# Kernel tuning notes

Hardware: AMD Instinct MI355X
Metric: run time of the kernel (lower is better)

## Reference

```python
import jax, jax.numpy as jnp
import numpy as np

T = 2048; HIDDEN = 2048; HQ = 32; G = 2; D = 64
KERNEL = 32; STRIDE = 16; BLOCK = 64; TOPK = 16
INIT_BLOCKS = 1; LOCAL_BLOCKS = 2; WINDOW = 512
ROPE_BASE = 10000.0
NEG = -1e30


def _rope(x):
    # x: [T, H, D], non-interleaved rotate-half rope
    t, h, d = x.shape
    half = d // 2
    inv = 1.0 / (ROPE_BASE ** (jnp.arange(half, dtype=jnp.float32) / half))
    freqs = jnp.arange(t, dtype=jnp.float32)[:, None] * inv[None, :]
    cos = jnp.cos(freqs)[:, None, :]
    sin = jnp.sin(freqs)[:, None, :]
    x1, x2 = x[..., :half], x[..., half:]
    return jnp.concatenate([x1 * cos - x2 * sin, x2 * cos + x1 * sin], axis=-1)


def setup_inputs() -> dict:
    key = jax.random.key(0)
    ks = jax.random.split(key, 8)
    s = 0.02
    return {
        "hidden_states": jax.random.normal(ks[0], (1, T, HIDDEN), jnp.float32),
        "Wq": jax.random.normal(ks[1], (HQ * D, HIDDEN), jnp.float32) * s,
        "Wk": jax.random.normal(ks[2], (G * D, HIDDEN), jnp.float32) * s,
        "Wv": jax.random.normal(ks[3], (G * D, HIDDEN), jnp.float32) * s,
        "Wo": jax.random.normal(ks[4], (HIDDEN, HQ * D), jnp.float32) * s,
        "Wgate": jax.random.normal(ks[5], (3, HIDDEN), jnp.float32) * s,
        "compress_key": jax.random.normal(ks[6], (G, D * KERNEL, D), jnp.float32) * s,
        "compress_value": jax.random.normal(ks[7], (G, D * KERNEL, D), jnp.float32) * s,
    }


def reference(hidden_states, Wq, Wk, Wv, Wo, Wgate, compress_key, compress_value):
    x = hidden_states[0]                      # [T, HIDDEN] (single varlen sequence)
    scale = 1.0 / np.sqrt(D).astype(np.float32)
    q = (x @ Wq.T).reshape(T, HQ, D)
    k = (x @ Wk.T).reshape(T, G, D)
    v = (x @ Wv.T).reshape(T, G, D)
    gate = jax.nn.sigmoid(x @ Wgate.T)        # [T, 3]
    q = _rope(q)
    k = _rope(k)

    # --- branch 1: compressed attention (linear_compress + compressed_attention) ---
    C = (T - KERNEL) // STRIDE + 1            # compressed sequence length
    starts = jnp.arange(C) * STRIDE
    win_idx = starts[:, None] + jnp.arange(KERNEL)[None, :]        # [C, KERNEL]
    kw = k[win_idx].transpose(2, 0, 1, 3).reshape(G, C, KERNEL * D)
    vw = v[win_idx].transpose(2, 0, 1, 3).reshape(G, C, KERNEL * D)
    ck = jnp.einsum('gcf,gfd->cgd', kw, compress_key)              # [C, G, D]
    cv = jnp.einsum('gcf,gfd->cgd', vw, compress_value)

    qg = q.reshape(T, G, HQ // G, D)          # [T, G, group, D]
    cs = jnp.einsum('tghd,cgd->ghtc', qg, ck) * scale              # [G, grp, T, C]
    # query i may attend compressed token j iff i >= j*stride + kernel - 1
    cmask = jnp.arange(T)[:, None] >= (starts + KERNEL - 1)[None, :]  # [T, C]
    cs = jnp.where(cmask[None, None], cs, NEG)
    p = jax.nn.softmax(cs, axis=-1)
    valid = cmask.any(-1)                     # queries with >=1 compressed key
    p = jnp.where(valid[None, None, :, None], p, 0.0)
    comp_out = jnp.einsum('ghtc,cgd->tghd', p, cv).reshape(T, HQ, D)

    # --- topk block selection from pooled compressed attention scores ---
    NB = T // BLOCK
    bstart = jnp.arange(NB) * BLOCK
    # compressed token j overlaps key block b
    overlap = ((starts[:, None] < bstart[None, :] + BLOCK) &
               (starts[:, None] + KERNEL > bstart[None, :])).astype(p.dtype)  # [C, NB]
    score = jnp.einsum('ghtc,cb->gtb', p, overlap)                 # [G, T, NB]
    qblock = jnp.arange(T) // BLOCK
    b = jnp.arange(NB)
    causal_b = b[None, :] <= qblock[:, None]                       # [T, NB]
    forced = (b[None, :] < INIT_BLOCKS) | (((qblock[:, None] - b[None, :]) < LOCAL_BLOCKS) & causal_b)
    score = jnp.where(forced[None], jnp.inf, score)
    score = jnp.where(causal_b[None], score, -jnp.inf)
    _, topk_idx = jax.lax.top_k(score, TOPK)                       # [G, T, TOPK]
    tk_valid = jnp.take_along_axis(score, topk_idx, axis=-1) > -jnp.inf
    sel = ((topk_idx[..., None] == b) & tk_valid[..., None]).any(axis=2)  # [G, T, NB]

    # --- branch 2: topk block-sparse attention ---
    key_block = jnp.arange(T) // BLOCK
    keymask = sel[:, :, key_block]                                 # [G, T, Tk]
    causal = jnp.arange(T)[:, None] >= jnp.arange(T)[None, :]      # [T, Tk]
    smask = keymask & causal[None]
    ss = jnp.einsum('tghd,sgd->ghts', qg, k) * scale               # [G, grp, T, Tk]
    ss = jnp.where(smask[:, None], ss, NEG)
    sparse_out = jnp.einsum('ghts,sgd->tghd', jax.nn.softmax(ss, -1), v).reshape(T, HQ, D)

    # --- branch 3: sliding window attention (causal, left window) ---
    delta = jnp.arange(T)[:, None] - jnp.arange(T)[None, :]
    wmask = (delta >= 0) & (delta <= WINDOW)                       # [T, Tk]
    ws = jnp.einsum('tghd,sgd->ghts', qg, k) * scale
    ws = jnp.where(wmask[None, None], ws, NEG)
    slide_out = jnp.einsum('ghts,sgd->tghd', jax.nn.softmax(ws, -1), v).reshape(T, HQ, D)

    # --- learned gate fusion + output projection ---
    out = (gate[:, 0, None, None] * comp_out +
           gate[:, 1, None, None] * sparse_out +
           gate[:, 2, None, None] * slide_out)                    # [T, HQ, D]
    o = out.reshape(T, HQ * D) @ Wo.T
    return o[None]                                                 # [1, T, HIDDEN]
```

## Files before the change

### kernel.cpp

```cpp
#include <hip/hip_runtime.h>
#include <math.h>

#define T_SEQ 2048
#define NHQ 32
#define NG 2
#define HD 64
#define CSTRIDE 16
#define KVGW 384

typedef __attribute__((ext_vector_type(8))) short short8_t;
typedef __attribute__((ext_vector_type(4))) short short4_t;
typedef __attribute__((ext_vector_type(4))) float f32x4;

__device__ __forceinline__ ushort f2bf(float x) {
  union { float f; unsigned u; } c; c.f = x;
  unsigned r = c.u + 0x7fff + ((c.u >> 16) & 1);
  return (ushort)(r >> 16);
}
__device__ __forceinline__ float bf2f(ushort u) {
  union { unsigned u; float f; } c; c.u = ((unsigned)u) << 16;
  return c.f;
}

__device__ __forceinline__ void glds16(const ushort* g, ushort* l) {
  __builtin_amdgcn_global_load_lds(
      (const __attribute__((address_space(1))) unsigned int*)g,
      (__attribute__((address_space(3))) unsigned int*)l, 16, 0, 0);
}

__global__ __launch_bounds__(256) void mgemm(
    const ushort* __restrict__ A, const ushort* __restrict__ B,
    float* __restrict__ C, int M, int N, int K) {
  __shared__ __align__(16) ushort As[128 * 64];
  __shared__ __align__(16) ushort Bs[64 * 64];
  const int tid = threadIdx.x;
  const int lane = tid & 63, w = tid >> 6;
  const int quad = lane >> 4, l16 = lane & 15;
  const int m0 = blockIdx.y * 128, n0 = blockIdx.x * 64;
  const int mq = (w & 1) * 64, nq = (w >> 1) * 32;
  f32x4 acc[4][2];
  const f32x4 fz = {0.f, 0.f, 0.f, 0.f};
  #pragma unroll
  for (int i = 0; i < 4; ++i)
    #pragma unroll
    for (int j = 0; j < 2; ++j) acc[i][j] = fz;

  for (int k0 = 0; k0 < K; k0 += 64) {
    __syncthreads();
    #pragma unroll
    for (int j = 0; j < 4; ++j) {
      int ci = j * 256 + tid;
      int row = ci >> 3, cl = ci & 7;
      int kc = cl ^ (row & 7);
      glds16(A + ((size_t)(m0 + row) * K + k0 + kc * 8), &As[ci * 8]);
    }
    #pragma unroll
    for (int j = 0; j < 2; ++j) {
      int ci = j * 256 + tid;
      int row = ci >> 3, cl = ci & 7;
      int kc = cl ^ (row & 7);
      glds16(B + ((size_t)(n0 + row) * K + k0 + kc * 8), &Bs[ci * 8]);
    }
    __syncthreads();
    #pragma unroll
    for (int kt = 0; kt < 2; ++kt) {
      short8_t af[4], bf_[2];
      #pragma unroll
      for (int mt = 0; mt < 4; ++mt) {
        int row = mq + mt * 16 + l16;
        int cl = (kt * 4 + quad) ^ (row & 7);
        af[mt] = *(const short8_t*)&As[row * 64 + cl * 8];
      }
      #pragma unroll
      for (int nt = 0; nt < 2; ++nt) {
        int row = nq + nt * 16 + l16;
        int cl = (kt * 4 + quad) ^ (row & 7);
        bf_[nt] = *(const short8_t*)&Bs[row * 64 + cl * 8];
      }
      #pragma unroll
      for (int mt = 0; mt < 4; ++mt)
        #pragma unroll
        for (int nt = 0; nt < 2; ++nt)
          acc[mt][nt] = __builtin_amdgcn_mfma_f32_16x16x32_bf16(
              af[mt], bf_[nt], acc[mt][nt], 0, 0, 0);
    }
  }
  #pragma unroll
  for (int mt = 0; mt < 4; ++mt)
    #pragma unroll
    for (int nt = 0; nt < 2; ++nt)
      #pragma unroll
      for (int r = 0; r < 4; ++r) {
        int m = m0 + mq + mt * 16 + quad * 4 + r;
        int n = n0 + nq + nt * 16 + l16;
        C[(size_t)m * N + n] = acc[mt][nt][r];
      }
}

__global__ __launch_bounds__(256) void cvt_bf(const float* __restrict__ src,
                                              ushort* __restrict__ dst, int n) {
  int i = (blockIdx.x * 256 + threadIdx.x) * 4;
  if (i >= n) return;
  float4 v = *(const float4*)(src + i);
  short4_t o = {(short)f2bf(v.x), (short)f2bf(v.y),
                (short)f2bf(v.z), (short)f2bf(v.w)};
  *(short4_t*)(dst + i) = o;
}

__global__ __launch_bounds__(256) void cvt_sum2_bf(const float* __restrict__ a,
                                                   const float* __restrict__ b,
                                                   ushort* __restrict__ dst, int n) {
  int i = (blockIdx.x * 256 + threadIdx.x) * 4;
  if (i >= n) return;
  float4 va = *(const float4*)(a + i);
  float4 vb = *(const float4*)(b + i);
  short4_t o = {(short)f2bf(va.x + vb.x), (short)f2bf(va.y + vb.y),
                (short)f2bf(va.z + vb.z), (short)f2bf(va.w + vb.w)};
  *(short4_t*)(dst + i) = o;
}

__global__ __launch_bounds__(256) void pack_wkvg(
    const float* __restrict__ Wk, const float* __restrict__ Wv,
    const float* __restrict__ Wg, ushort* __restrict__ dst) {
  int i = blockIdx.x * 256 + threadIdx.x;
  if (i >= KVGW * 2048) return;
  int n = i >> 11, k = i & 2047;
  float v;
  if (n < 128) v = Wk[(size_t)n * 2048 + k];
  else if (n < 256) v = Wv[(size_t)(n - 128) * 2048 + k];
  else if (n < 259) v = Wg[(size_t)(n - 256) * 2048 + k];
  else v = 0.f;
  dst[i] = f2bf(v);
}

__global__ __launch_bounds__(256) void cvt_vt(const float* __restrict__ kvg,
                                              ushort* __restrict__ vt) {
  int i = blockIdx.x * 256 + threadIdx.x;
  if (i >= T_SEQ * NG * HD) return;
  int d = i & 63, g = (i >> 6) & 1, s = i >> 7;
  int blk = s >> 6, k = s & 63;
  int snew = blk * 64 + (((k >> 2) ^ (d & 15)) << 2) + (k & 3);
  vt[((size_t)g * HD + d) * T_SEQ + snew] =
      f2bf(kvg[(size_t)s * KVGW + 128 + g * 64 + d]);
}

__global__ __launch_bounds__(256) void rope_all(
    const float* __restrict__ q, float* __restrict__ kvg,
    ushort* __restrict__ qbf, ushort* __restrict__ kbf) {
  const int t = blockIdx.x;
  const float lnb_over = 9.210340371976184f / 32.f;
  for (int job = threadIdx.x; job < (NHQ + NG) * 32; job += 256) {
    int h = job >> 5, j = job & 31;
    float inv = expf(-(float)j * lnb_over);
    float fr = (float)t * inv;
    float c_ = cosf(fr), s_ = sinf(fr);
    if (h < NHQ) {
      const float cq = c_ * 0.125f, sq = s_ * 0.125f;
      const float* base = q + ((size_t)t * NHQ + h) * HD;
      float x1 = base[j], x2 = base[j + 32];
      ushort* ob = qbf + ((size_t)t * NHQ + h) * HD;
      ob[j] = f2bf(x1 * cq - x2 * sq);
      ob[j + 32] = f2bf(x2 * cq + x1 * sq);
    } else {
      int g = h - NHQ;
      float* base = kvg + (size_t)t * KVGW + g * 64;
      float x1 = base[j], x2 = base[j + 32];
      float o1 = x1 * c_ - x2 * s_, o2 = x2 * c_ + x1 * s_;
      base[j] = o1; base[j + 32] = o2;
      kbf[(size_t)t * 128 + g * 64 + j] = f2bf(o1);
      kbf[(size_t)t * 128 + g * 64 + j + 32] = f2bf(o2);
    }
  }
}

__global__ __launch_bounds__(256) void compress_kv(
    const float* __restrict__ kvg,
    const float* __restrict__ Wck, const float* __restrict__ Wcv,
    ushort* __restrict__ ck16, ushort* __restrict__ cvt16) {
  const int c = blockIdx.x, g = blockIdx.y;
  const int tid = threadIdx.x;
  if (c == 127) {
    if (tid < 64) ck16[((size_t)127 * NG + g) * HD + tid] = 0;
    else if (tid < 128) cvt16[((size_t)g * HD + (tid - 64)) * 128 + 127] = 0;
    return;
  }
  const int d = tid & 63, chunk = tid >> 6;
  __shared__ float red[2][4][64];
  float ak = 0.f, av = 0.f;
  #pragma unroll 4
  for (int f = chunk * 512; f < chunk * 512 + 512; ++f) {
    int i = f >> 6, e = f & 63;
    int trow = c * CSTRIDE + i;
    float kv = kvg[(size_t)trow * KVGW + g * 64 + e];
    float vv = kvg[(size_t)trow * KVGW + 128 + g * 64 + e];
    ak += kv * Wck[((size_t)g * 2048 + f) * HD + d];
    av += vv * Wcv[((size_t)g * 2048 + f) * HD + d];
  }
  red[0][chunk][d] = ak;
  red[1][chunk][d] = av;
  __syncthreads();
  if (tid < 64) {
    ck16[((size_t)c * NG + g) * HD + tid] =
        f2bf(red[0][0][tid] + red[0][1][tid] + red[0][2][tid] + red[0][3][tid]);
  } else if (tid < 128) {
    int dd = tid - 64;
    cvt16[((size_t)g * HD + dd) * 128 + c] =
        f2bf(red[1][0][dd] + red[1][1][dd] + red[1][2][dd] + red[1][3][dd]);
  }
}

__global__ __launch_bounds__(512) void comp_attn(
    const ushort* __restrict__ qbf, const ushort* __restrict__ ck16,
    const ushort* __restrict__ cvt16, const float* __restrict__ kvg,
    float* __restrict__ comb, unsigned* __restrict__ sel) {
  const int tb = 127 - blockIdx.x, g = blockIdx.y;
  const int t0 = tb * 16;
  const int tid = threadIdx.x, lane = tid & 63, w = tid >> 6;
  const int quad = lane >> 4, l16 = lane & 15;
  const int qb = t0 >> 6;

  __shared__ float colsum[16][129];
  for (int i = tid; i < 16 * 129; i += 512) ((float*)colsum)[i] = 0.f;
  __syncthreads();

  const int t = t0 + l16;
  const int cmaxv = (t >= 31) ? min(126, (t - 31) >> 4) : -1;
  const int h0 = w * 2;

  short8_t qB[2][2];
  #pragma unroll
  for (int hh = 0; hh < 2; ++hh)
    #pragma unroll
    for (int kd = 0; kd < 2; ++kd)
      qB[hh][kd] = *(const short8_t*)(qbf +
          ((size_t)t * NHQ + g * 16 + h0 + hh) * HD + kd * 32 + quad * 8);

  const f32x4 fz = {0.f, 0.f, 0.f, 0.f};
  f32x4 sp[2][8];

  #pragma unroll
  for (int ct = 0; ct < 8; ++ct) {
    const ushort* kr = ck16 + ((size_t)(ct * 16 + l16) * NG + g) * HD + quad * 8;
    short8_t kA0 = *(const short8_t*)kr;
    short8_t kA1 = *(const short8_t*)(kr + 32);
    #pragma unroll
    for (int hh = 0; hh < 2; ++hh) {
      f32x4 c0 = __builtin_amdgcn_mfma_f32_16x16x32_bf16(kA0, qB[hh][0], fz, 0, 0, 0);
      sp[hh][ct] = __builtin_amdgcn_mfma_f32_16x16x32_bf16(kA1, qB[hh][1], c0, 0, 0, 0);
    }
  }

  short4_t pB[2][8];
  #pragma unroll
  for (int hh = 0; hh < 2; ++hh) {
    float mx = -INFINITY;
    #pragma unroll
    for (int ct = 0; ct < 8; ++ct)
      #pragma unroll
      for (int r = 0; r < 4; ++r) {
        int c = ct * 16 + quad * 4 + r;
        float s_ = (c <= cmaxv) ? sp[hh][ct][r] : -INFINITY;
        sp[hh][ct][r] = s_;
        mx = fmaxf(mx, s_);
      }
    mx = fmaxf(mx, __shfl_xor(mx, 16));
    mx = fmaxf(mx, __shfl_xor(mx, 32));
    if (mx == -INFINITY) mx = 0.f;
    float ls = 0.f;
    #pragma unroll
    for (int ct = 0; ct < 8; ++ct)
      #pragma unroll
      for (int r = 0; r < 4; ++r) {
        float p = __expf(sp[hh][ct][r] - mx);
        sp[hh][ct][r] = p;
        ls += p;
      }
    ls += __shfl_xor(ls, 16);
    ls += __shfl_xor(ls, 32);
    float inv = (ls > 0.f) ? 1.f / ls : 0.f;
    #pragma unroll
    for (int ct = 0; ct < 8; ++ct) {
      short4_t pk;
      #pragma unroll
      for (int r = 0; r < 4; ++r) {
        float pn = sp[hh][ct][r] * inv;
        sp[hh][ct][r] = pn;
        pk[r] = (short)f2bf(pn);
      }
      pB[hh][ct] = pk;
    }
  }

  #pragma unroll
  for (int ct = 0; ct < 8; ++ct)
    #pragma unroll
    for (int r = 0; r < 4; ++r)
      atomicAdd(&colsum[l16][ct * 16 + quad * 4 + r],
                sp[0][ct][r] + sp[1][ct][r]);

  f32x4 acc[2][4];
  #pragma unroll
  for (int hh = 0; hh < 2; ++hh)
    #pragma unroll
    for (int dt = 0; dt < 4; ++dt) acc[hh][dt] = fz;
  #pragma unroll
  for (int ct = 0; ct < 8; ++ct) {
    short4_t vA[4];
    #pragma unroll
    for (int dt = 0; dt < 4; ++dt)
      vA[dt] = *(const short4_t*)(cvt16 +
          ((size_t)g * HD + dt * 16 + l16) * 128 + ct * 16 + quad * 4);
    #pragma unroll
    for (int hh = 0; hh < 2; ++hh)
      #pragma unroll
      for (int dt = 0; dt < 4; ++dt)
        acc[hh][dt] = __builtin_amdgcn_mfma_f32_16x16x16bf16_1k(
            vA[dt], pB[hh][ct], acc[hh][dt], 0, 0, 0);
  }

  const float g0 = 1.f / (1.f + __expf(-kvg[(size_t)t * KVGW + 256]));
  #pragma unroll
  for (int hh = 0; hh < 2; ++hh)
    #pragma unroll
    for (int dt = 0; dt < 4; ++dt)
      #pragma unroll
      for (int r = 0; r < 4; ++r)
        comb[((size_t)t * NHQ + g * 16 + h0 + hh) * HD + dt * 16 + quad * 4 + r] =
            g0 * acc[hh][dt][r];

  __syncthreads();

  {
    const int tl = tid >> 5;
    const int b = tid & 31;
    float s;
    if (b > qb) s = -INFINITY;
    else if (b == 0 || qb - b < 2) s = INFINITY;
    else {
      s = 0.f;
      #pragma unroll
      for (int i = 0; i < 5; ++i) s += colsum[tl][4 * b - 1 + i];
    }
    unsigned key = (s < 0.f) ? 0u : (__float_as_uint(s) + 1u);
    unsigned msel = 0;
    for (int it = 0; it < 16; ++it) {
      unsigned long long pk =
          (((unsigned long long)key) << 6) | (unsigned)(63 - b);
      #pragma unroll
      for (int off = 16; off >= 1; off >>= 1) {
        unsigned long long o = __shfl_xor(pk, off);
        if (o > pk) pk = o;
      }
      if ((pk >> 6) == 0) break;
      int bs = 63 - (int)(pk & 63);
      msel |= 1u << bs;
      if (b == bs) key = 0;
    }
    if (b == 0) sel[(size_t)(t0 + tl) * NG + g] = msel;
  }
}

__global__ __launch_bounds__(512, 2) void mfma_attn(
    const ushort* __restrict__ qb16, const ushort* __restrict__ kb16,
    const ushort* __restrict__ vtb, const float* __restrict__ kvg,
    const unsigned* __restrict__ sel, float* __restrict__ comb2) {
  const int qb = 31 - blockIdx.x, g = blockIdx.y;
  const int hgp = blockIdx.z;
  const int tid = threadIdx.x, lane = tid & 63, w = tid >> 6;
  const int quad = lane >> 4, l16 = lane & 15;
  const int head = g * 16 + hgp * 2 + (w >> 2);
  const int t0 = qb * 64;

  __shared__ __align__(16) ushort Ks[2][64 * 64];
  __shared__ __align__(16) ushort Vs[2][64 * 64];
  __shared__ unsigned sel_s[64];

  if (tid < 64) sel_s[tid] = sel[(size_t)(t0 + tid) * NG + g];
  __syncthreads();

  const int qg = t0 + (w & 3) * 16 + l16;
  const unsigned sbq = sel_s[(w & 3) * 16 + l16];

  short8_t qB0 = *(const short8_t*)(qb16 +
      ((size_t)qg * NHQ + head) * HD + quad * 8);
  short8_t qB1 = *(const short8_t*)(qb16 +
      ((size_t)qg * NHQ + head) * HD + 32 + quad * 8);

  float m0 = -1e30f, m1 = -1e30f;
  f32x4 acc0[4], acc1[4], accL0, accL1;
  const f32x4 fz = {0.f, 0.f, 0.f, 0.f};
  #pragma unroll
  for (int dt = 0; dt < 4; ++dt) { acc0[dt] = fz; acc1[dt] = fz; }
  accL0 = fz; accL1 = fz;
  const short4_t onesA = {(short)0x3F80, (short)0x3F80,
                          (short)0x3F80, (short)0x3F80};

  unsigned uni = sel_s[lane];
  #pragma unroll
  for (int off = 32; off >= 1; off >>= 1) uni |= __shfl_xor(uni, off);
  const int b0w = (qb > 8) ? qb - 8 : 0;
  const unsigned wmask = ((1u << (qb - b0w + 1)) - 1u) << b0w;
  unsigned lrem = uni | wmask;
  const int nb = __popc(lrem);

  #define STAGE(buf, blk)                                                     \
    {                                                                         \
      const int blk_ = (blk);                                                 \
      const int row = tid >> 3, cl = tid & 7;                                 \
      const int kck = cl ^ (row & 7);                                         \
      glds16(kb16 + (size_t)(blk_ * 64 + row) * 128 + g * 64 + kck * 8,       \
             &Ks[buf][tid * 8]);                                              \
      glds16(vtb + ((size_t)g * 64 + row) * 2048 + blk_ * 64 + cl * 8,        \
             &Vs[buf][tid * 8]);                                              \
    }

  int blkcur = __ffs(lrem) - 1; lrem &= lrem - 1;
  STAGE(0, blkcur);
  __syncthreads();

  const int e = l16 & 7;

  for (int ib = 0; ib < nb; ++ib) {
    const int cur = ib & 1;
    const int blk = blkcur;
    if (ib + 1 < nb) {
      blkcur = __ffs(lrem) - 1; lrem &= lrem - 1;
      STAGE(cur ^ 1, blkcur);
    }

    f32x4 sp[4];
    __builtin_amdgcn_s_setprio(1);
    #pragma unroll
    for (int kt = 0; kt < 4; ++kt) {
      const ushort* kr = &Ks[cur][(kt * 16 + l16) * 64];
      short8_t kA0 = *(const short8_t*)(kr + ((quad ^ e) * 8));
      short8_t kA1 = *(const short8_t*)(kr + ((quad ^ e ^ 4) * 8));
      f32x4 c = __builtin_amdgcn_mfma_f32_16x16x32_bf16(kA0, qB0, fz, 0, 0, 0);
      sp[kt] = __builtin_amdgcn_mfma_f32_16x16x32_bf16(kA1, qB1, c, 0, 0, 0);
    }
    __builtin_amdgcn_s_setprio(0);

    const bool diag = (blk == qb);
    const bool wedge = (blk == qb - 8);
    const bool inU = ((uni >> blk) & 1u) != 0;
    const bool inW = ((wmask >> blk) & 1u) != 0;
    const bool selq = ((sbq >> blk) & 1u) != 0;

    float rm = -INFINITY;
    #pragma unroll
    for (int kt = 0; kt < 4; ++kt)
      #pragma unroll
      for (int r = 0; r < 4; ++r) rm = fmaxf(rm, sp[kt][r]);
    rm = fmaxf(rm, __shfl_xor(rm, 16));
    rm = fmaxf(rm, __shfl_xor(rm, 32));

    if (inU) {
      float mx;
      if (!diag) {
        mx = selq ? rm : -INFINITY;
      } else {
        mx = -INFINITY;
        #pragma unroll
        for (int kt = 0; kt < 4; ++kt)
          #pragma unroll
          for (int r = 0; r < 4; ++r) {
            int key = blk * 64 + kt * 16 + quad * 4 + r;
            bool ok = selq && (key <= qg);
            mx = ok ? fmaxf(mx, sp[kt][r]) : mx;
          }
        mx = fmaxf(mx, __shfl_xor(mx, 16));
        mx = fmaxf(mx, __shfl_xor(mx, 32));
      }
      if (!__all(mx <= m0 + 8.f)) {
        float mnew = fmaxf(m0, mx);
        float alpha = __expf(m0 - mnew);
        #pragma unroll
        for (int dt = 0; dt < 4; ++dt)
          #pragma unroll
          for (int r = 0; r < 4; ++r) acc0[dt][r] *= alpha;
        #pragma unroll
        for (int r = 0; r < 4; ++r) accL0[r] *= alpha;
        m0 = mnew;
      }
      short4_t pB[4];
      #pragma unroll
      for (int kt = 0; kt < 4; ++kt) {
        union { unsigned u[2]; short4_t s; } pk;
        if (!diag) {
          float p0 = __expf(sp[kt][0] - m0), p1 = __expf(sp[kt][1] - m0);
          float p2 = __expf(sp[kt][2] - m0), p3 = __expf(sp[kt][3] - m0);
          asm("v_cvt_pk_bf16_f32 %0, %1, %2" : "=v"(pk.u[0]) : "v"(p0), "v"(p1));
          asm("v_cvt_pk_bf16_f32 %0, %1, %2" : "=v"(pk.u[1]) : "v"(p2), "v"(p3));
          pk.u[0] = selq ? pk.u[0] : 0u;
          pk.u[1] = selq ? pk.u[1] : 0u;
        } else {
          float p[4];
          #pragma unroll
          for (int r = 0; r < 4; ++r) {
            int key = blk * 64 + kt * 16 + quad * 4 + r;
            bool ok = selq && (key <= qg);
            p[r] = ok ? __expf(sp[kt][r] - m0) : 0.f;
          }
          asm("v_cvt_pk_bf16_f32 %0, %1, %2" : "=v"(pk.u[0]) : "v"(p[0]), "v"(p[1]));
          asm("v_cvt_pk_bf16_f32 %0, %1, %2" : "=v"(pk.u[1]) : "v"(p[2]), "v"(p[3]));
        }
        pB[kt] = pk.s;
      }
      __builtin_amdgcn_s_setprio(1);
      #pragma unroll
      for (int kt = 0; kt < 4; ++kt) {
        #pragma unroll
        for (int dt = 0; dt < 4; ++dt) {
          short4_t vA = *(const short4_t*)(&Vs[cur][(dt * 16 + l16) * 64 +
                                                    (((kt * 4 + quad) ^ l16) << 2)]);
          acc0[dt] = __builtin_amdgcn_mfma_f32_16x16x16bf16_1k(
              vA, pB[kt], acc0[dt], 0, 0, 0);
        }
        accL0 = __builtin_amdgcn_mfma_f32_16x16x16bf16_1k(
            onesA, pB[kt], accL0, 0, 0, 0);
      }
      __builtin_amdgcn_s_setprio(0);
    }

    if (inW) {
      float mx;
      if (!diag && !wedge) {
        mx = rm;
      } else {
        mx = -INFINITY;
        #pragma unroll
        for (int kt = 0; kt < 4; ++kt)
          #pragma unroll
          for (int r = 0; r < 4; ++r) {
            int key = blk * 64 + kt * 16 + quad * 4 + r;
            bool ok = (key <= qg) && (qg - key <= 512);
            mx = ok ? fmaxf(mx, sp[kt][r]) : mx;
          }
        mx = fmaxf(mx, __shfl_xor(mx, 16));
        mx = fmaxf(mx, __shfl_xor(mx, 32));
      }
      if (!__all(mx <= m1 + 8.f)) {
        float mnew = fmaxf(m1, mx);
        float alpha = __expf(m1 - mnew);
        #pragma unroll
        for (int dt = 0; dt < 4; ++dt)
          #pragma unroll
          for (int r = 0; r < 4; ++r) acc1[dt][r] *= alpha;
        #pragma unroll
        for (int r = 0; r < 4; ++r) accL1[r] *= alpha;
        m1 = mnew;
      }
      short4_t pB[4];
      #pragma unroll
      for (int kt = 0; kt < 4; ++kt) {
        union { unsigned u[2]; short4_t s; } pk;
        if (!diag && !wedge) {
          float p0 = __expf(sp[kt][0] - m1), p1 = __expf(sp[kt][1] - m1);
          float p2 = __expf(sp[kt][2] - m1), p3 = __expf(sp[kt][3] - m1);
          asm("v_cvt_pk_bf16_f32 %0, %1, %2" : "=v"(pk.u[0]) : "v"(p0), "v"(p1));
          asm("v_cvt_pk_bf16_f32 %0, %1, %2" : "=v"(pk.u[1]) : "v"(p2), "v"(p3));
        } else {
          float p[4];
          #pragma unroll
          for (int r = 0; r < 4; ++r) {
            int key = blk * 64 + kt * 16 + quad * 4 + r;
            bool ok = (key <= qg) && (qg - key <= 512);
            p[r] = ok ? __expf(sp[kt][r] - m1) : 0.f;
          }
          asm("v_cvt_pk_bf16_f32 %0, %1, %2" : "=v"(pk.u[0]) : "v"(p[0]), "v"(p[1]));
          asm("v_cvt_pk_bf16_f32 %0, %1, %2" : "=v"(pk.u[1]) : "v"(p[2]), "v"(p[3]));
        }
        pB[kt] = pk.s;
      }
      __builtin_amdgcn_s_setprio(1);
      #pragma unroll
      for (int kt = 0; kt < 4; ++kt) {
        #pragma unroll
        for (int dt = 0; dt < 4; ++dt) {
          short4_t vA = *(const short4_t*)(&Vs[cur][(dt * 16 + l16) * 64 +
                                                    (((kt * 4 + quad) ^ l16) << 2)]);
          acc1[dt] = __builtin_amdgcn_mfma_f32_16x16x16bf16_1k(
              vA, pB[kt], acc1[dt], 0, 0, 0);
        }
        accL1 = __builtin_amdgcn_mfma_f32_16x16x16bf16_1k(
            onesA, pB[kt], accL1, 0, 0, 0);
      }
      __builtin_amdgcn_s_setprio(0);
    }

    __syncthreads();
  }
  #undef STAGE

  const float c0 =
      (1.f / (1.f + __expf(-kvg[(size_t)qg * KVGW + 257]))) / accL0[0];
  const float c1 =
      (1.f / (1.f + __expf(-kvg[(size_t)qg * KVGW + 258]))) / accL1[0];
  #pragma unroll
  for (int dt = 0; dt < 4; ++dt)
    #pragma unroll
    for (int r = 0; r < 4; ++r) {
      const int d = dt * 16 + quad * 4 + r;
      comb2[((size_t)qg * NHQ + head) * HD + d] =
          c0 * acc0[dt][r] + c1 * acc1[dt][r];
    }
}

extern "C" void kernel_launch(void* const* d_in, const int* in_sizes, int n_in,
                              void* d_out, int out_size, void* d_ws, size_t ws_size,
                              hipStream_t stream) {
  const float* x   = (const float*)d_in[0];
  const float* Wq  = (const float*)d_in[1];
  const float* Wk  = (const float*)d_in[2];
  const float* Wv  = (const float*)d_in[3];
  const float* Wo  = (const float*)d_in[4];
  const float* Wg  = (const float*)d_in[5];
  const float* Wck = (const float*)d_in[6];
  const float* Wcv = (const float*)d_in[7];
  float* out = (float*)d_out;
  float* ws = (float*)d_ws;

  float* qbuf   = ws;
  float* comb1  = qbuf + 4194304;
  float* kvg    = comb1 + 4194304;
  float* ckb    = kvg + 786432;
  float* cvb    = ckb + 16384;
  unsigned* sel = (unsigned*)(cvb + 16384);
  ushort* kbf   = (ushort*)(sel + 4096);
  ushort* vtb   = kbf + 262144;
  ushort* wkvgb = vtb + 262144;
  ushort* regA  = wkvgb + 786432;
  ushort* regB  = regA + 4194304;
  ushort* xb = regA;      ushort* combb = regA;
  ushort* wqb = regB;     ushort* qbf = regB;
  float* comb2 = qbuf;
  ushort* wob = (ushort*)qbuf;

  ushort* ckb16 = (ushort*)ckb;
  ushort* cvtb  = ckb16 + 16384;

  const int CV4 = (1048576 + 255) / 256;
  cvt_bf<<<CV4, 256, 0, stream>>>(x, xb, 4194304);
  cvt_bf<<<CV4, 256, 0, stream>>>(Wq, wqb, 4194304);
  pack_wkvg<<<(KVGW * 2048 + 255) / 256, 256, 0, stream>>>(Wk, Wv, Wg, wkvgb);

  mgemm<<<dim3(32, 16), 256, 0, stream>>>(xb, wqb, qbuf, 2048, 2048, 2048);
  mgemm<<<dim3(6, 16), 256, 0, stream>>>(xb, wkvgb, kvg, 2048, KVGW, 2048);

  rope_all<<<2048, 256, 0, stream>>>(qbuf, kvg, qbf, kbf);
  cvt_vt<<<(262144 + 255) / 256, 256, 0, stream>>>(kvg, vtb);
  compress_kv<<<dim3(128, 2), 256, 0, stream>>>(kvg, Wck, Wcv, ckb16, cvtb);
  comp_attn<<<dim3(128, 2), 512, 0, stream>>>(qbf, ckb16, cvtb, kvg, comb1, sel);
  mfma_attn<<<dim3(32, 2, 8), 512, 0, stream>>>(qbf, kbf, vtb, kvg, sel, comb2);

  cvt_sum2_bf<<<CV4, 256, 0, stream>>>(comb1, comb2, combb, 4194304);
  cvt_bf<<<CV4, 256, 0, stream>>>(Wo, wob, 4194304);
  mgemm<<<dim3(32, 16), 256, 0, stream>>>(combb, wob, out, 2048, 2048, 2048);
}
```

Before: 378.6 us.

## Fuse comb sum and bf16 cast into attention epilogue; use exp2 softmax

The attention kernel now reads the compressed-branch output, adds its own gated result and writes the bf16 combined tensor directly, which removes the separate cvt_sum2_bf pass and the fp32 comb2 round trip. The query scale is folded with log2(e) so every softmax exponent becomes exp2f, and the rescale threshold is widened to match the base-2 scale. The Wo conversion moves earlier in the stream, and half the head groups process query blocks in ascending order to balance causal work. The wider threshold slightly raises the risk of larger unnormalised accumulators.

```diff
diff --git a/kernel.cpp b/kernel.cpp
--- a/kernel.cpp
+++ b/kernel.cpp
@@ -107,18 +107,6 @@
   *(short4_t*)(dst + i) = o;
 }
 
-__global__ __launch_bounds__(256) void cvt_sum2_bf(const float* __restrict__ a,
-                                                   const float* __restrict__ b,
-                                                   ushort* __restrict__ dst, int n) {
-  int i = (blockIdx.x * 256 + threadIdx.x) * 4;
-  if (i >= n) return;
-  float4 va = *(const float4*)(a + i);
-  float4 vb = *(const float4*)(b + i);
-  short4_t o = {(short)f2bf(va.x + vb.x), (short)f2bf(va.y + vb.y),
-                (short)f2bf(va.z + vb.z), (short)f2bf(va.w + vb.w)};
-  *(short4_t*)(dst + i) = o;
-}
-
 __global__ __launch_bounds__(256) void pack_wkvg(
     const float* __restrict__ Wk, const float* __restrict__ Wv,
     const float* __restrict__ Wg, ushort* __restrict__ dst) {
@@ -149,13 +137,14 @@
     ushort* __restrict__ qbf, ushort* __restrict__ kbf) {
   const int t = blockIdx.x;
   const float lnb_over = 9.210340371976184f / 32.f;
+  const float QS = 0.18033688011112042f;
   for (int job = threadIdx.x; job < (NHQ + NG) * 32; job += 256) {
     int h = job >> 5, j = job & 31;
     float inv = expf(-(float)j * lnb_over);
     float fr = (float)t * inv;
     float c_ = cosf(fr), s_ = sinf(fr);
     if (h < NHQ) {
-      const float cq = c_ * 0.125f, sq = s_ * 0.125f;
+      const float cq = c_ * QS, sq = s_ * QS;
       const float* base = q + ((size_t)t * NHQ + h) * HD;
       float x1 = base[j], x2 = base[j + 32];
       ushort* ob = qbf + ((size_t)t * NHQ + h) * HD;
@@ -271,7 +260,7 @@
     for (int ct = 0; ct < 8; ++ct)
       #pragma unroll
       for (int r = 0; r < 4; ++r) {
-        float p = __expf(sp[hh][ct][r] - mx);
+        float p = exp2f(sp[hh][ct][r] - mx);
         sp[hh][ct][r] = p;
         ls += p;
       }
@@ -363,9 +352,11 @@
 __global__ __launch_bounds__(512, 2) void mfma_attn(
     const ushort* __restrict__ qb16, const ushort* __restrict__ kb16,
     const ushort* __restrict__ vtb, const float* __restrict__ kvg,
-    const unsigned* __restrict__ sel, float* __restrict__ comb2) {
-  const int qb = 31 - blockIdx.x, g = blockIdx.y;
+    const unsigned* __restrict__ sel, const float* __restrict__ comb1,
+    ushort* __restrict__ combb) {
+  const int g = blockIdx.y;
   const int hgp = blockIdx.z;
+  const int qb = (hgp >= 4) ? blockIdx.x : 31 - blockIdx.x;
   const int tid = threadIdx.x, lane = tid & 63, w = tid >> 6;
   const int quad = lane >> 4, l16 = lane & 15;
   const int head = g * 16 + hgp * 2 + (w >> 2);
@@ -471,9 +462,9 @@
         mx = fmaxf(mx, __shfl_xor(mx, 16));
         mx = fmaxf(mx, __shfl_xor(mx, 32));
       }
-      if (!__all(mx <= m0 + 8.f)) {
+      if (!__all(mx <= m0 + 11.f)) {
         float mnew = fmaxf(m0, mx);
-        float alpha = __expf(m0 - mnew);
+        float alpha = exp2f(m0 - mnew);
         #pragma unroll
         for (int dt = 0; dt < 4; ++dt)
           #pragma unroll
@@ -487,8 +478,8 @@
       for (int kt = 0; kt < 4; ++kt) {
         union { unsigned u[2]; short4_t s; } pk;
         if (!diag) {
-          float p0 = __expf(sp[kt][0] - m0), p1 = __expf(sp[kt][1] - m0);
-          float p2 = __expf(sp[kt][2] - m0), p3 = __expf(sp[kt][3] - m0);
+          float p0 = exp2f(sp[kt][0] - m0), p1 = exp2f(sp[kt][1] - m0);
+          float p2 = exp2f(sp[kt][2] - m0), p3 = exp2f(sp[kt][3] - m0);
           asm("v_cvt_pk_bf16_f32 %0, %1, %2" : "=v"(pk.u[0]) : "v"(p0), "v"(p1));
           asm("v_cvt_pk_bf16_f32 %0, %1, %2" : "=v"(pk.u[1]) : "v"(p2), "v"(p3));
           pk.u[0] = selq ? pk.u[0] : 0u;
@@ -499,7 +490,7 @@
           for (int r = 0; r < 4; ++r) {
             int key = blk * 64 + kt * 16 + quad * 4 + r;
             bool ok = selq && (key <= qg);
-            p[r] = ok ? __expf(sp[kt][r] - m0) : 0.f;
+            p[r] = ok ? exp2f(sp[kt][r] - m0) : 0.f;
           }
           asm("v_cvt_pk_bf16_f32 %0, %1, %2" : "=v"(pk.u[0]) : "v"(p[0]), "v"(p[1]));
           asm("v_cvt_pk_bf16_f32 %0, %1, %2" : "=v"(pk.u[1]) : "v"(p[2]), "v"(p[3]));
@@ -539,9 +530,9 @@
         mx = fmaxf(mx, __shfl_xor(mx, 16));
         mx = fmaxf(mx, __shfl_xor(mx, 32));
       }
-      if (!__all(mx <= m1 + 8.f)) {
+      if (!__all(mx <= m1 + 11.f)) {
         float mnew = fmaxf(m1, mx);
-        float alpha = __expf(m1 - mnew);
+        float alpha = exp2f(m1 - mnew);
         #pragma unroll
         for (int dt = 0; dt < 4; ++dt)
           #pragma unroll
@@ -555,8 +546,8 @@
       for (int kt = 0; kt < 4; ++kt) {
         union { unsigned u[2]; short4_t s; } pk;
         if (!diag && !wedge) {
-          float p0 = __expf(sp[kt][0] - m1), p1 = __expf(sp[kt][1] - m1);
-          float p2 = __expf(sp[kt][2] - m1), p3 = __expf(sp[kt][3] - m1);
+          float p0 = exp2f(sp[kt][0] - m1), p1 = exp2f(sp[kt][1] - m1);
+          float p2 = exp2f(sp[kt][2] - m1), p3 = exp2f(sp[kt][3] - m1);
           asm("v_cvt_pk_bf16_f32 %0, %1, %2" : "=v"(pk.u[0]) : "v"(p0), "v"(p1));
           asm("v_cvt_pk_bf16_f32 %0, %1, %2" : "=v"(pk.u[1]) : "v"(p2), "v"(p3));
         } else {
@@ -565,7 +556,7 @@
           for (int r = 0; r < 4; ++r) {
             int key = blk * 64 + kt * 16 + quad * 4 + r;
             bool ok = (key <= qg) && (qg - key <= 512);
-            p[r] = ok ? __expf(sp[kt][r] - m1) : 0.f;
+            p[r] = ok ? exp2f(sp[kt][r] - m1) : 0.f;
           }
           asm("v_cvt_pk_bf16_f32 %0, %1, %2" : "=v"(pk.u[0]) : "v"(p[0]), "v"(p[1]));
           asm("v_cvt_pk_bf16_f32 %0, %1, %2" : "=v"(pk.u[1]) : "v"(p[2]), "v"(p[3]));
@@ -597,13 +588,15 @@
   const float c1 =
       (1.f / (1.f + __expf(-kvg[(size_t)qg * KVGW + 258]))) / accL1[0];
   #pragma unroll
-  for (int dt = 0; dt < 4; ++dt)
-    #pragma unroll
-    for (int r = 0; r < 4; ++r) {
-      const int d = dt * 16 + quad * 4 + r;
-      comb2[((size_t)qg * NHQ + head) * HD + d] =
-          c0 * acc0[dt][r] + c1 * acc1[dt][r];
-    }
+  for (int dt = 0; dt < 4; ++dt) {
+    const size_t base = ((size_t)qg * NHQ + head) * HD + dt * 16 + quad * 4;
+    f32x4 cv = *(const f32x4*)(comb1 + base);
+    short4_t o;
+    #pragma unroll
+    for (int r = 0; r < 4; ++r)
+      o[r] = (short)f2bf(cv[r] + c0 * acc0[dt][r] + c1 * acc1[dt][r]);
+    *(short4_t*)(combb + base) = o;
+  }
 }
 
 extern "C" void kernel_launch(void* const* d_in, const int* in_sizes, int n_in,
@@ -633,7 +626,6 @@
   ushort* regB  = regA + 4194304;
   ushort* xb = regA;      ushort* combb = regA;
   ushort* wqb = regB;     ushort* qbf = regB;
-  float* comb2 = qbuf;
   ushort* wob = (ushort*)qbuf;
 
   ushort* ckb16 = (ushort*)ckb;
@@ -648,12 +640,11 @@
   mgemm<<<dim3(6, 16), 256, 0, stream>>>(xb, wkvgb, kvg, 2048, KVGW, 2048);
 
   rope_all<<<2048, 256, 0, stream>>>(qbuf, kvg, qbf, kbf);
+  cvt_bf<<<CV4, 256, 0, stream>>>(Wo, wob, 4194304);
   cvt_vt<<<(262144 + 255) / 256, 256, 0, stream>>>(kvg, vtb);
   compress_kv<<<dim3(128, 2), 256, 0, stream>>>(kvg, Wck, Wcv, ckb16, cvtb);
   comp_attn<<<dim3(128, 2), 512, 0, stream>>>(qbf, ckb16, cvtb, kvg, comb1, sel);
-  mfma_attn<<<dim3(32, 2, 8), 512, 0, stream>>>(qbf, kbf, vtb, kvg, sel, comb2);
-
-  cvt_sum2_bf<<<CV4, 256, 0, stream>>>(comb1, comb2, combb, 4194304);
-  cvt_bf<<<CV4, 256, 0, stream>>>(Wo, wob, 4194304);
+  mfma_attn<<<dim3(32, 2, 8), 512, 0, stream>>>(qbf, kbf, vtb, kvg, sel, comb1, combb);
+
   mgemm<<<dim3(32, 16), 256, 0, stream>>>(combb, wob, out, 2048, 2048, 2048);
 }
```

Measured after the change: 371.3 us. About the same (-1.9%).
